# Kernel tuning notes

Measured on AMD Instinct MI355X. Metric: run time of the kernel, lower is better.

The kernel has to match this reference:

```python
import jax, jax.numpy as jnp
import numpy as np

N_NODES = 100000
N_EDGES = 1600000
IN_DIM = 256
HEAD_DIM = 64  # out_dim // num_heads = 256 // 4
NEG_SLOPE = 0.01  # F.leaky_relu default


def setup_inputs() -> dict:
    key = jax.random.key(0)
    k1, k2, k3, k4, k5, k6 = jax.random.split(key, 6)
    h = jax.random.normal(k1, (N_NODES, IN_DIM), dtype=jnp.float32)
    snorm_n = jax.random.uniform(k2, (N_NODES, 1), dtype=jnp.float32)
    fc_w = jax.random.normal(k3, (HEAD_DIM, IN_DIM), dtype=jnp.float32) * (1.0 / np.sqrt(IN_DIM))
    attn_w = jax.random.normal(k4, (1, 2 * HEAD_DIM), dtype=jnp.float32) * (1.0 / np.sqrt(2 * HEAD_DIM))
    src = jax.random.randint(k5, (N_EDGES,), 0, N_NODES, dtype=jnp.int64 if jax.config.jax_enable_x64 else jnp.int32)
    dst = jax.random.randint(k6, (N_EDGES,), 0, N_NODES, dtype=jnp.int64 if jax.config.jax_enable_x64 else jnp.int32)
    return {"h": h, "snorm_n": snorm_n, "fc_w": fc_w, "attn_w": attn_w, "src": src, "dst": dst}


def reference(h, snorm_n, fc_w, attn_w, src, dst):
    N = h.shape[0]
    z = h @ fc_w.T  # [N, d]
    d = z.shape[1]
    # attn_fc(cat([z_src, z_dst])) == z_src @ w_l + z_dst @ w_r
    w_l, w_r = attn_w[0, :d], attn_w[0, d:]
    el = z @ w_l  # [N]
    er = z @ w_r  # [N]
    e = jax.nn.leaky_relu(el[src] + er[dst], NEG_SLOPE)  # [E] edge scores
    # segment softmax over incoming edges of each dst node
    m = jax.ops.segment_max(e, dst, num_segments=N)
    m = jnp.where(jnp.isfinite(m), m, 0.0)  # empty segments -> -inf, neutralize
    ex = jnp.exp(e - m[dst])
    denom = jax.ops.segment_sum(ex, dst, num_segments=N)
    alpha = ex / denom[dst]  # [E]
    # weighted scatter-sum of source features
    h_out = jax.ops.segment_sum(alpha[:, None] * z[src], dst, num_segments=N)  # [N, d]
    h_out = h_out * snorm_n  # graph_norm
    return jax.nn.relu(h_out)
```

## Files before the change

kernel.cpp:

```cpp
#include <hip/hip_runtime.h>
#include <math.h>

#define NEG_SLOPE 0.01f
#define NB 256
#define BATCH 4096
#define GEMM_BLOCKS 2048
#define HPAD 260

typedef __attribute__((ext_vector_type(8))) short short8;
typedef __attribute__((ext_vector_type(4))) float f32x4;

__device__ __forceinline__ unsigned short f2bf_rne(float f) {
    unsigned u = __float_as_uint(f);
    unsigned r = 0x7fffu + ((u >> 16) & 1u);
    return (unsigned short)((u + r) >> 16);
}
__device__ __forceinline__ float bf2f(unsigned short b) {
    return __uint_as_float(((unsigned)b) << 16);
}
__device__ __forceinline__ unsigned cvtpk(float lo, float hi) {
    unsigned r;
    asm("v_cvt_pk_bf16_f32 %0, %1, %2" : "=v"(r) : "v"(lo), "v"(hi));
    return r;
}
__device__ __forceinline__ short8 pack8(float4 a, float4 b) {
    union { unsigned u[4]; short8 s; } r;
    r.u[0] = cvtpk(a.x, a.y);
    r.u[1] = cvtpk(a.z, a.w);
    r.u[2] = cvtpk(b.x, b.y);
    r.u[3] = cvtpk(b.z, b.w);
    return r.s;
}

__global__ __launch_bounds__(256) void k_hist(
    const int* __restrict__ dst, int* __restrict__ hist_blk, int n_edges,
    const float* __restrict__ fc_w,
    unsigned short* __restrict__ w_hi, unsigned short* __restrict__ w_lo, int wdim)
{
    const int tid = threadIdx.x;
    const int nbatch = (n_edges + BATCH - 1) / BATCH;
    if ((int)blockIdx.x < nbatch) {
        __shared__ int hist[NB];
        const int batch = blockIdx.x;
        hist[tid] = 0;
        __syncthreads();
        const int e0 = batch * BATCH;
        const int n = min(BATCH, n_edges - e0);
        #pragma unroll
        for (int k = 0; k < 16; ++k) {
            int j = tid + k * 256;
            if (j < n) atomicAdd(&hist[dst[e0 + j] >> 9], 1);
        }
        __syncthreads();
        hist_blk[batch * NB + tid] = hist[tid];
    } else {
        int i = (blockIdx.x - nbatch) * 256 + tid;
        if (i < wdim) {
            float f = fc_w[i];
            unsigned u = __float_as_uint(f);
            w_hi[i] = (unsigned short)(u >> 16);
            float lo = f - __uint_as_float(u & 0xffff0000u);
            w_lo[i] = f2bf_rne(lo);
        }
    }
}

__global__ __launch_bounds__(256) void k_p2loc(
    const int* __restrict__ hist_blk, int* __restrict__ bb,
    int* __restrict__ bucket_tot, int n_edges)
{
    const int tid = threadIdx.x;
    const int b = blockIdx.x;
    const int nbatch = (n_edges + BATCH - 1) / BATCH;
    __shared__ int v[512], s2[256];
    v[tid]       = (tid < nbatch)       ? hist_blk[tid * NB + b]         : 0;
    v[tid + 256] = (tid + 256 < nbatch) ? hist_blk[(tid + 256) * NB + b] : 0;
    __syncthreads();
    int pair = v[2 * tid] + v[2 * tid + 1];
    s2[tid] = pair;
    __syncthreads();
    for (int off = 1; off < 256; off <<= 1) {
        int t = (tid >= off) ? s2[tid - off] : 0;
        __syncthreads();
        s2[tid] += t;
        __syncthreads();
    }
    int e2 = s2[tid] - pair;
    if (2 * tid < nbatch)     bb[b * nbatch + 2 * tid]     = e2;
    if (2 * tid + 1 < nbatch) bb[b * nbatch + 2 * tid + 1] = e2 + v[2 * tid];
    if (tid == 255) bucket_tot[b] = s2[255];
}

__global__ __launch_bounds__(256) void k_p2a(
    const int* __restrict__ bucket_tot, int* __restrict__ bucket_base)
{
    const int tid = threadIdx.x;
    __shared__ int a[NB];
    int tot = bucket_tot[tid];
    a[tid] = tot;
    __syncthreads();
    for (int off = 1; off < NB; off <<= 1) {
        int t = (tid >= off) ? a[tid - off] : 0;
        __syncthreads();
        a[tid] += t;
        __syncthreads();
    }
    bucket_base[tid] = a[tid] - tot;
    if (tid == NB - 1) bucket_base[NB] = a[tid];
}

__global__ __launch_bounds__(256) void k_p3convgemm(
    const int* __restrict__ src, const int* __restrict__ dst,
    const int* __restrict__ bb, const int* __restrict__ bucket_base,
    unsigned* __restrict__ rec1, int n_edges,
    const float* __restrict__ h,
    const unsigned short* __restrict__ w_hi, const unsigned short* __restrict__ w_lo,
    const float* __restrict__ attn_w,
    unsigned short* __restrict__ z_bf16, float* __restrict__ el, float* __restrict__ er,
    int n_nodes)
{
    __shared__ __align__(16) char smem[32 * HPAD * 4 + 1024];
    const int tid = threadIdx.x;
    const int nbatch = (n_edges + BATCH - 1) / BATCH;

    if ((int)blockIdx.x < nbatch) {
        int* hist  = (int*)smem;
        int* offs  = hist + NB;
        int* cnt2  = offs + NB;
        int* gbase = cnt2 + NB;
        unsigned* staged = (unsigned*)(gbase + NB);
        unsigned char* sbkt = (unsigned char*)(staged + BATCH);
        const int batch = blockIdx.x;
        const int e0 = batch * BATCH;
        const int n = min(BATCH, n_edges - e0);
        hist[tid] = 0; cnt2[tid] = 0;
        gbase[tid] = bucket_base[tid] + bb[tid * nbatch + batch];
        __syncthreads();
        int d[16], s[16];
        #pragma unroll
        for (int k = 0; k < 16; ++k) {
            int j = tid + k * 256;
            if (j < n) {
                d[k] = dst[e0 + j];
                s[k] = src[e0 + j];
                atomicAdd(&hist[d[k] >> 9], 1);
            } else d[k] = -1;
        }
        __syncthreads();
        int hv = hist[tid];
        for (int off = 1; off < NB; off <<= 1) {
            int t = (tid >= off) ? hist[tid - off] : 0;
            __syncthreads();
            hist[tid] += t;
            __syncthreads();
        }
        offs[tid] = hist[tid] - hv;
        __syncthreads();
        #pragma unroll
        for (int k = 0; k < 16; ++k) {
            if (d[k] >= 0) {
                int b = d[k] >> 9;
                int r = atomicAdd(&cnt2[b], 1);
                int slot = offs[b] + r;
                staged[slot] = ((unsigned)(d[k] & 511) << 17) | (unsigned)s[k];
                sbkt[slot] = (unsigned char)b;
            }
        }
        __syncthreads();
        #pragma unroll
        for (int k = 0; k < 16; ++k) {
            int j = tid + k * 256;
            if (j < n) {
                int b = sbkt[j];
                rec1[gbase[b] + (j - offs[b])] = staged[j];
            }
        }
    } else {
        float* hstage = (float*)smem;
        float* elp = hstage + 32 * HPAD;
        float* erp = elp + 4 * 32;
        const int vbid  = blockIdx.x - nbatch;
        const int vgrid = gridDim.x - nbatch;
        const int lane = tid & 63;
        const int wave = tid >> 6;
        const int c    = lane & 15;
        const int g    = lane >> 4;
        const int c0   = wave * 16;

        short8 bh[8], bl[8];
        #pragma unroll
        for (int t = 0; t < 8; ++t) {
            const int koff = (c0 + c) * 256 + t * 32 + g * 8;
            bh[t] = *(const short8*)(w_hi + koff);
            bl[t] = *(const short8*)(w_lo + koff);
        }
        const float wl_lane = attn_w[c0 + c];
        const float wr_lane = attn_w[64 + c0 + c];

        const int ntiles = (n_nodes + 31) >> 5;
        for (int tile = vbid; tile < ntiles; tile += vgrid) {
            const int n0 = tile << 5;
            float4 sv[8];
            #pragma unroll
            for (int rr = 0; rr < 8; ++rr) {
                int ridx = min(n0 + wave * 8 + rr, n_nodes - 1);
                sv[rr] = *(const float4*)(h + (size_t)ridx * 256 + lane * 4);
            }
            #pragma unroll
            for (int rr = 0; rr < 8; ++rr)
                *(float4*)&hstage[(wave * 8 + rr) * HPAD + lane * 4] = sv[rr];
            __syncthreads();

            short8 a0[8], a1[8];
            #pragma unroll
            for (int t = 0; t < 8; ++t) {
                const float* p0 = &hstage[c * HPAD + t * 32 + g * 8];
                const float* p1 = &hstage[(c + 16) * HPAD + t * 32 + g * 8];
                float4 x0 = *(const float4*)p0;
                float4 x1 = *(const float4*)(p0 + 4);
                float4 y0 = *(const float4*)p1;
                float4 y1 = *(const float4*)(p1 + 4);
                a0[t] = pack8(x0, x1);
                a1[t] = pack8(y0, y1);
            }
            f32x4 acc0 = {0.f, 0.f, 0.f, 0.f};
            f32x4 acc1 = {0.f, 0.f, 0.f, 0.f};
            #pragma unroll
            for (int t = 0; t < 8; ++t) {
                acc0 = __builtin_amdgcn_mfma_f32_16x16x32_bf16(a0[t], bh[t], acc0, 0, 0, 0);
                acc1 = __builtin_amdgcn_mfma_f32_16x16x32_bf16(a1[t], bh[t], acc1, 0, 0, 0);
                acc0 = __builtin_amdgcn_mfma_f32_16x16x32_bf16(a0[t], bl[t], acc0, 0, 0, 0);
                acc1 = __builtin_amdgcn_mfma_f32_16x16x32_bf16(a1[t], bl[t], acc1, 0, 0, 0);
            }
            #pragma unroll
            for (int j = 0; j < 4; ++j) {
                int ra = n0 + 4 * g + j;
                int rb = ra + 16;
                if (ra < n_nodes) z_bf16[(size_t)ra * 64 + c0 + c] = f2bf_rne(acc0[j]);
                if (rb < n_nodes) z_bf16[(size_t)rb * 64 + c0 + c] = f2bf_rne(acc1[j]);
            }
            float pl0[4], pr0[4], pl1[4], pr1[4];
            #pragma unroll
            for (int j = 0; j < 4; ++j) {
                pl0[j] = acc0[j] * wl_lane; pr0[j] = acc0[j] * wr_lane;
                pl1[j] = acc1[j] * wl_lane; pr1[j] = acc1[j] * wr_lane;
            }
            #pragma unroll
            for (int off = 1; off < 16; off <<= 1) {
                #pragma unroll
                for (int j = 0; j < 4; ++j) {
                    pl0[j] += __shfl_xor(pl0[j], off);
                    pr0[j] += __shfl_xor(pr0[j], off);
                    pl1[j] += __shfl_xor(pl1[j], off);
                    pr1[j] += __shfl_xor(pr1[j], off);
                }
            }
            if (c == 0) {
                #pragma unroll
                for (int j = 0; j < 4; ++j) {
                    elp[wave * 32 + 4 * g + j]      = pl0[j];
                    elp[wave * 32 + 16 + 4 * g + j] = pl1[j];
                    erp[wave * 32 + 4 * g + j]      = pr0[j];
                    erp[wave * 32 + 16 + 4 * g + j] = pr1[j];
                }
            }
            __syncthreads();
            if (tid < 32) {
                if (n0 + tid < n_nodes)
                    el[n0 + tid] = elp[tid] + elp[32 + tid] + elp[64 + tid] + elp[96 + tid];
            } else if (tid < 64) {
                int r = tid - 32;
                if (n0 + r < n_nodes)
                    er[n0 + r] = erp[r] + erp[32 + r] + erp[64 + r] + erp[96 + r];
            }
            __syncthreads();
        }
    }
}

__global__ __launch_bounds__(256) void k_p4(
    const unsigned* __restrict__ rec1, const int* __restrict__ bucket_base,
    const float* __restrict__ el, const float* __restrict__ er,
    int* __restrict__ rowstart, int2* __restrict__ rec,
    int n_nodes, int n_edges)
{
    const int tid = threadIdx.x;
    const int b = blockIdx.x;
    const int beg  = bucket_base[b];
    const int endb = bucket_base[b + 1];
    const int nbuse = (n_nodes + 511) >> 9;
    __shared__ int cnt[512], offs[512], s2[256];
    cnt[tid] = 0; cnt[tid + 256] = 0;
    __syncthreads();
    for (int i = beg + tid; i < endb; i += 256)
        atomicAdd(&cnt[rec1[i] >> 17], 1);
    __syncthreads();
    int pair = cnt[2 * tid] + cnt[2 * tid + 1];
    s2[tid] = pair;
    __syncthreads();
    for (int off = 1; off < 256; off <<= 1) {
        int t = (tid >= off) ? s2[tid - off] : 0;
        __syncthreads();
        s2[tid] += t;
        __syncthreads();
    }
    int e2 = s2[tid] - pair;
    offs[2 * tid]     = e2;
    offs[2 * tid + 1] = e2 + cnt[2 * tid];
    __syncthreads();
    for (int t2 = tid; t2 < 512; t2 += 256) {
        int node = (b << 9) + t2;
        if (node < n_nodes) rowstart[node] = beg + offs[t2];
    }
    if (b == nbuse - 1 && tid == 0) rowstart[n_nodes] = n_edges;
    cnt[tid] = 0; cnt[tid + 256] = 0;
    __syncthreads();
    for (int i = beg + tid; i < endb; i += 256) {
        unsigned u = rec1[i];
        int rd = (int)(u >> 17);
        int s  = (int)(u & 0x1FFFFu);
        int r = atomicAdd(&cnt[rd], 1);
        float ev = el[s] + er[(b << 9) + rd];
        ev = (ev > 0.f) ? ev : NEG_SLOPE * ev;
        rec[beg + offs[rd] + r] = make_int2(s, __float_as_int(ev));
    }
}

__global__ __launch_bounds__(256) void k_agg(
    const int* __restrict__ rowstart, const int2* __restrict__ rec,
    const unsigned short* __restrict__ z,
    const float* __restrict__ snorm, float* __restrict__ out, int n_nodes)
{
    const int wid  = (blockIdx.x * blockDim.x + threadIdx.x) >> 6;
    const int lane = threadIdx.x & 63;
    if (wid >= n_nodes) return;
    const int t = lane & 15;
    const int g = lane >> 4;
    const int start = rowstart[wid];
    const int end   = rowstart[wid + 1];
    if (end == start) {
        if (g == 0) *(float4*)(out + (size_t)wid * 64 + t * 4) = make_float4(0.f, 0.f, 0.f, 0.f);
        return;
    }
    float denom = 0.f;
    float acc0 = 0.f, acc1 = 0.f, acc2 = 0.f, acc3 = 0.f;
    const int last = end - 1;
    for (int ib = start; ib < end; ib += 8) {
        int iA = ib + g;
        int iB = ib + 4 + g;
        bool vA = iA < end, vB = iB < end;
        int2 eA = rec[min(iA, last)];
        int2 eB = rec[min(iB, last)];
        ushort4 za = *(const ushort4*)(z + (size_t)eA.x * 64 + t * 4);
        ushort4 zb = *(const ushort4*)(z + (size_t)eB.x * 64 + t * 4);
        float wA = vA ? __expf(__int_as_float(eA.y)) : 0.f;
        float wB = vB ? __expf(__int_as_float(eB.y)) : 0.f;
        denom += wA + wB;
        acc0 = fmaf(wA, bf2f(za.x), acc0);
        acc1 = fmaf(wA, bf2f(za.y), acc1);
        acc2 = fmaf(wA, bf2f(za.z), acc2);
        acc3 = fmaf(wA, bf2f(za.w), acc3);
        acc0 = fmaf(wB, bf2f(zb.x), acc0);
        acc1 = fmaf(wB, bf2f(zb.y), acc1);
        acc2 = fmaf(wB, bf2f(zb.z), acc2);
        acc3 = fmaf(wB, bf2f(zb.w), acc3);
    }
    #pragma unroll
    for (int off = 16; off <= 32; off <<= 1) {
        denom += __shfl_xor(denom, off);
        acc0  += __shfl_xor(acc0,  off);
        acc1  += __shfl_xor(acc1,  off);
        acc2  += __shfl_xor(acc2,  off);
        acc3  += __shfl_xor(acc3,  off);
    }
    if (g == 0) {
        float s = snorm[wid] / denom;
        float4 o;
        o.x = fmaxf(acc0 * s, 0.f);
        o.y = fmaxf(acc1 * s, 0.f);
        o.z = fmaxf(acc2 * s, 0.f);
        o.w = fmaxf(acc3 * s, 0.f);
        *(float4*)(out + (size_t)wid * 64 + t * 4) = o;
    }
}

extern "C" void kernel_launch(void* const* d_in, const int* in_sizes, int n_in,
                              void* d_out, int out_size, void* d_ws, size_t ws_size,
                              hipStream_t stream)
{
    const float* h      = (const float*)d_in[0];
    const float* snorm  = (const float*)d_in[1];
    const float* fc_w   = (const float*)d_in[2];
    const float* attn_w = (const float*)d_in[3];
    const int*   src    = (const int*)d_in[4];
    const int*   dst    = (const int*)d_in[5];
    float* out = (float*)d_out;

    const int n_nodes = in_sizes[1];
    const int n_edges = in_sizes[4];
    const int wdim    = in_sizes[2];
    const int nbatch  = (n_edges + BATCH - 1) / BATCH;
    const int nprep   = (wdim + 255) / 256;

    char* wsp = (char*)d_ws;
    size_t off = 0;
    auto alloc = [&](size_t bytes) -> void* {
        void* p = wsp + off;
        off += (bytes + 255) & ~(size_t)255;
        return p;
    };
    unsigned short* z_bf16 = (unsigned short*)alloc((size_t)n_nodes * 64 * sizeof(unsigned short));
    unsigned short* w_hi   = (unsigned short*)alloc((size_t)wdim * sizeof(unsigned short));
    unsigned short* w_lo   = (unsigned short*)alloc((size_t)wdim * sizeof(unsigned short));
    float* el        = (float*)alloc((size_t)n_nodes * sizeof(float));
    float* er        = (float*)alloc((size_t)n_nodes * sizeof(float));
    int*   hist_blk  = (int*)  alloc((size_t)nbatch * NB * sizeof(int));
    int*   bucket_tot  = (int*)alloc((size_t)NB * sizeof(int));
    int*   bucket_base = (int*)alloc((size_t)(NB + 1) * sizeof(int));
    int*   bb        = (int*)  alloc((size_t)NB * nbatch * sizeof(int));
    int*   rowstart  = (int*)  alloc(((size_t)n_nodes + 1) * sizeof(int));
    unsigned* rec1   = (unsigned*)alloc((size_t)n_edges * sizeof(unsigned));
    int2*  rec       = (int2*) alloc((size_t)n_edges * sizeof(int2));

    k_hist<<<nbatch + nprep, 256, 0, stream>>>(
        dst, hist_blk, n_edges, fc_w, w_hi, w_lo, wdim);
    k_p2loc<<<NB, 256, 0, stream>>>(hist_blk, bb, bucket_tot, n_edges);
    k_p2a<<<1, 256, 0, stream>>>(bucket_tot, bucket_base);
    k_p3convgemm<<<nbatch + GEMM_BLOCKS, 256, 0, stream>>>(
        src, dst, bb, bucket_base, rec1, n_edges,
        h, w_hi, w_lo, attn_w, z_bf16, el, er, n_nodes);
    k_p4<<<NB, 256, 0, stream>>>(rec1, bucket_base, el, er, rowstart, rec,
                                 n_nodes, n_edges);
    k_agg<<<((size_t)n_nodes * 64 + 255) / 256, 256, 0, stream>>>(
        rowstart, rec, z_bf16, snorm, out, n_nodes);
}
```

Measured before the change: 130.3 us.

## Launch one GEMM block per node tile and stage h as bf16 in LDS

The fused conversion/GEMM kernel changes from a persistent grid-stride loop over 2048 blocks to one block per 32-node tile, so the grid grows to about 3125 GEMM blocks. Rows of h are converted to bf16 before being written to shared memory, which halves LDS footprint and lets MFMA operands be read directly as short8 without repacking. The weight-fragment loads are moved after the h loads so they overlap. In exchange, every block reloads the W fragments and attention weights, and there are more blocks to launch and schedule.

```diff
diff --git a/kernel.cpp b/kernel.cpp
--- a/kernel.cpp
+++ b/kernel.cpp
@@ -4,8 +4,7 @@
 #define NEG_SLOPE 0.01f
 #define NB 256
 #define BATCH 4096
-#define GEMM_BLOCKS 2048
-#define HPAD 260
+#define HROW 264
 
 typedef __attribute__((ext_vector_type(8))) short short8;
 typedef __attribute__((ext_vector_type(4))) float f32x4;
@@ -22,14 +21,6 @@
     unsigned r;
     asm("v_cvt_pk_bf16_f32 %0, %1, %2" : "=v"(r) : "v"(lo), "v"(hi));
     return r;
-}
-__device__ __forceinline__ short8 pack8(float4 a, float4 b) {
-    union { unsigned u[4]; short8 s; } r;
-    r.u[0] = cvtpk(a.x, a.y);
-    r.u[1] = cvtpk(a.z, a.w);
-    r.u[2] = cvtpk(b.x, b.y);
-    r.u[3] = cvtpk(b.z, b.w);
-    return r.s;
 }
 
 __global__ __launch_bounds__(256) void k_hist(
@@ -119,7 +110,7 @@
     unsigned short* __restrict__ z_bf16, float* __restrict__ el, float* __restrict__ er,
     int n_nodes)
 {
-    __shared__ __align__(16) char smem[32 * HPAD * 4 + 1024];
+    __shared__ __align__(16) char smem[24832];
     const int tid = threadIdx.x;
     const int nbatch = (n_edges + BATCH - 1) / BATCH;
 
@@ -176,17 +167,30 @@
             }
         }
     } else {
-        float* hstage = (float*)smem;
-        float* elp = hstage + 32 * HPAD;
-        float* erp = elp + 4 * 32;
-        const int vbid  = blockIdx.x - nbatch;
-        const int vgrid = gridDim.x - nbatch;
+        unsigned short* hstage = (unsigned short*)smem;
+        float* elp = (float*)(smem + 32 * HROW * 2);
+        float* erp = elp + 128;
+        const int tile = blockIdx.x - nbatch;
         const int lane = tid & 63;
         const int wave = tid >> 6;
         const int c    = lane & 15;
         const int g    = lane >> 4;
         const int c0   = wave * 16;
 
+        const int n0 = tile << 5;
+        float4 sv[8];
+        #pragma unroll
+        for (int rr = 0; rr < 8; ++rr) {
+            int ridx = min(n0 + wave * 8 + rr, n_nodes - 1);
+            sv[rr] = *(const float4*)(h + (size_t)ridx * 256 + lane * 4);
+        }
+        #pragma unroll
+        for (int rr = 0; rr < 8; ++rr) {
+            unsigned lo = cvtpk(sv[rr].x, sv[rr].y);
+            unsigned hi = cvtpk(sv[rr].z, sv[rr].w);
+            *(uint2*)&hstage[(wave * 8 + rr) * HROW + lane * 4] = make_uint2(lo, hi);
+        }
+
         short8 bh[8], bl[8];
         #pragma unroll
         for (int t = 0; t < 8; ++t) {
@@ -196,84 +200,59 @@
         }
         const float wl_lane = attn_w[c0 + c];
         const float wr_lane = attn_w[64 + c0 + c];
-
-        const int ntiles = (n_nodes + 31) >> 5;
-        for (int tile = vbid; tile < ntiles; tile += vgrid) {
-            const int n0 = tile << 5;
-            float4 sv[8];
-            #pragma unroll
-            for (int rr = 0; rr < 8; ++rr) {
-                int ridx = min(n0 + wave * 8 + rr, n_nodes - 1);
-                sv[rr] = *(const float4*)(h + (size_t)ridx * 256 + lane * 4);
-            }
-            #pragma unroll
-            for (int rr = 0; rr < 8; ++rr)
-                *(float4*)&hstage[(wave * 8 + rr) * HPAD + lane * 4] = sv[rr];
-            __syncthreads();
-
-            short8 a0[8], a1[8];
-            #pragma unroll
-            for (int t = 0; t < 8; ++t) {
-                const float* p0 = &hstage[c * HPAD + t * 32 + g * 8];
-                const float* p1 = &hstage[(c + 16) * HPAD + t * 32 + g * 8];
-                float4 x0 = *(const float4*)p0;
-                float4 x1 = *(const float4*)(p0 + 4);
-                float4 y0 = *(const float4*)p1;
-                float4 y1 = *(const float4*)(p1 + 4);
-                a0[t] = pack8(x0, x1);
-                a1[t] = pack8(y0, y1);
-            }
-            f32x4 acc0 = {0.f, 0.f, 0.f, 0.f};
-            f32x4 acc1 = {0.f, 0.f, 0.f, 0.f};
-            #pragma unroll
-            for (int t = 0; t < 8; ++t) {
-                acc0 = __builtin_amdgcn_mfma_f32_16x16x32_bf16(a0[t], bh[t], acc0, 0, 0, 0);
-                acc1 = __builtin_amdgcn_mfma_f32_16x16x32_bf16(a1[t], bh[t], acc1, 0, 0, 0);
-                acc0 = __builtin_amdgcn_mfma_f32_16x16x32_bf16(a0[t], bl[t], acc0, 0, 0, 0);
-                acc1 = __builtin_amdgcn_mfma_f32_16x16x32_bf16(a1[t], bl[t], acc1, 0, 0, 0);
-            }
+        __syncthreads();
+
+        f32x4 acc0 = {0.f, 0.f, 0.f, 0.f};
+        f32x4 acc1 = {0.f, 0.f, 0.f, 0.f};
+        #pragma unroll
+        for (int t = 0; t < 8; ++t) {
+            short8 a0 = *(const short8*)&hstage[c * HROW + t * 32 + g * 8];
+            short8 a1 = *(const short8*)&hstage[(c + 16) * HROW + t * 32 + g * 8];
+            acc0 = __builtin_amdgcn_mfma_f32_16x16x32_bf16(a0, bh[t], acc0, 0, 0, 0);
+            acc1 = __builtin_amdgcn_mfma_f32_16x16x32_bf16(a1, bh[t], acc1, 0, 0, 0);
+            acc0 = __builtin_amdgcn_mfma_f32_16x16x32_bf16(a0, bl[t], acc0, 0, 0, 0);
+            acc1 = __builtin_amdgcn_mfma_f32_16x16x32_bf16(a1, bl[t], acc1, 0, 0, 0);
+        }
+        #pragma unroll
+        for (int j = 0; j < 4; ++j) {
+            int ra = n0 + 4 * g + j;
+            int rb = ra + 16;
+            if (ra < n_nodes) z_bf16[(size_t)ra * 64 + c0 + c] = f2bf_rne(acc0[j]);
+            if (rb < n_nodes) z_bf16[(size_t)rb * 64 + c0 + c] = f2bf_rne(acc1[j]);
+        }
+        float pl0[4], pr0[4], pl1[4], pr1[4];
+        #pragma unroll
+        for (int j = 0; j < 4; ++j) {
+            pl0[j] = acc0[j] * wl_lane; pr0[j] = acc0[j] * wr_lane;
+            pl1[j] = acc1[j] * wl_lane; pr1[j] = acc1[j] * wr_lane;
+        }
+        #pragma unroll
+        for (int off = 1; off < 16; off <<= 1) {
             #pragma unroll
             for (int j = 0; j < 4; ++j) {
-                int ra = n0 + 4 * g + j;
-                int rb = ra + 16;
-                if (ra < n_nodes) z_bf16[(size_t)ra * 64 + c0 + c] = f2bf_rne(acc0[j]);
-                if (rb < n_nodes) z_bf16[(size_t)rb * 64 + c0 + c] = f2bf_rne(acc1[j]);
+                pl0[j] += __shfl_xor(pl0[j], off);
+                pr0[j] += __shfl_xor(pr0[j], off);
+                pl1[j] += __shfl_xor(pl1[j], off);
+                pr1[j] += __shfl_xor(pr1[j], off);
             }
-            float pl0[4], pr0[4], pl1[4], pr1[4];
+        }
+        if (c == 0) {
             #pragma unroll
             for (int j = 0; j < 4; ++j) {
-                pl0[j] = acc0[j] * wl_lane; pr0[j] = acc0[j] * wr_lane;
-                pl1[j] = acc1[j] * wl_lane; pr1[j] = acc1[j] * wr_lane;
+                elp[wave * 32 + 4 * g + j]      = pl0[j];
+                elp[wave * 32 + 16 + 4 * g + j] = pl1[j];
+                erp[wave * 32 + 4 * g + j]      = pr0[j];
+                erp[wave * 32 + 16 + 4 * g + j] = pr1[j];
             }
-            #pragma unroll
-            for (int off = 1; off < 16; off <<= 1) {
-                #pragma unroll
-                for (int j = 0; j < 4; ++j) {
-                    pl0[j] += __shfl_xor(pl0[j], off);
-                    pr0[j] += __shfl_xor(pr0[j], off);
-                    pl1[j] += __shfl_xor(pl1[j], off);
-                    pr1[j] += __shfl_xor(pr1[j], off);
-                }
-            }
-            if (c == 0) {
-                #pragma unroll
-                for (int j = 0; j < 4; ++j) {
-                    elp[wave * 32 + 4 * g + j]      = pl0[j];
-                    elp[wave * 32 + 16 + 4 * g + j] = pl1[j];
-                    erp[wave * 32 + 4 * g + j]      = pr0[j];
-                    erp[wave * 32 + 16 + 4 * g + j] = pr1[j];
-                }
-            }
-            __syncthreads();
-            if (tid < 32) {
-                if (n0 + tid < n_nodes)
-                    el[n0 + tid] = elp[tid] + elp[32 + tid] + elp[64 + tid] + elp[96 + tid];
-            } else if (tid < 64) {
-                int r = tid - 32;
-                if (n0 + r < n_nodes)
-                    er[n0 + r] = erp[r] + erp[32 + r] + erp[64 + r] + erp[96 + r];
-            }
-            __syncthreads();
+        }
+        __syncthreads();
+        if (tid < 32) {
+            if (n0 + tid < n_nodes)
+                el[n0 + tid] = elp[tid] + elp[32 + tid] + elp[64 + tid] + elp[96 + tid];
+        } else if (tid < 64) {
+            int r = tid - 32;
+            if (n0 + r < n_nodes)
+                er[n0 + r] = erp[r] + erp[32 + r] + erp[64 + r] + erp[96 + r];
         }
     }
 }
@@ -401,6 +380,7 @@
     const int wdim    = in_sizes[2];
     const int nbatch  = (n_edges + BATCH - 1) / BATCH;
     const int nprep   = (wdim + 255) / 256;
+    const int ntiles  = (n_nodes + 31) >> 5;
 
     char* wsp = (char*)d_ws;
     size_t off = 0;
@@ -426,7 +406,7 @@
         dst, hist_blk, n_edges, fc_w, w_hi, w_lo, wdim);
     k_p2loc<<<NB, 256, 0, stream>>>(hist_blk, bb, bucket_tot, n_edges);
     k_p2a<<<1, 256, 0, stream>>>(bucket_tot, bucket_base);
-    k_p3convgemm<<<nbatch + GEMM_BLOCKS, 256, 0, stream>>>(
+    k_p3convgemm<<<nbatch + ntiles, 256, 0, stream>>>(
         src, dst, bb, bucket_base, rec1, n_edges,
         h, w_hi, w_lo, attn_w, z_bf16, el, er, n_nodes);
     k_p4<<<NB, 256, 0, stream>>>(rec1, bucket_base, el, er, rowstart, rec,
```

Result: no change. 128.1 us, median of 3 (-1.7%).
